# Performance work log

Measured on AMD Instinct MI355X. Metric: run time of the kernel, lower is better.

The kernel has to match this reference:

```python
import jax, jax.numpy as jnp
import numpy as np

POOL = 7        # output pooled size
SAMP = 2 * POOL # crop_and_resize sampling resolution (14)


def _bilinear_crop(feat, ys, xs):
    """feat [H,W,C]; ys,xs [N,S] sample coords in feature-map pixels -> [N,S,S,C]."""
    H, W, _ = feat.shape
    ys = jnp.clip(ys, 0.0, H - 1.0)
    xs = jnp.clip(xs, 0.0, W - 1.0)
    y0f = jnp.floor(ys); x0f = jnp.floor(xs)
    y0 = y0f.astype(jnp.int32); x0 = x0f.astype(jnp.int32)
    y1 = jnp.clip(y0 + 1, 0, H - 1); x1 = jnp.clip(x0 + 1, 0, W - 1)
    wy = (ys - y0f)[:, :, None, None]   # [N,S,1,1]
    wx = (xs - x0f)[:, None, :, None]   # [N,1,S,1]
    g = lambda yi, xi: feat[yi[:, :, None], xi[:, None, :]]  # [N,S,S,C]
    out = g(y0, x0) * (1 - wy) * (1 - wx)
    out = out + g(y0, x1) * (1 - wy) * wx
    out = out + g(y1, x0) * wy * (1 - wx)
    out = out + g(y1, x1) * wy * wx
    return out


def setup_inputs() -> dict:
    key = jax.random.key(0)
    k1, k2, k3, k4, k5 = jax.random.split(key, 5)
    Hf, Wf, C = 37, 50, 512
    N = 1000
    H_img, W_img = 600.0, 800.0
    inputs = jax.random.normal(k1, (1, Hf, Wf, C), dtype=jnp.float32)
    # random valid boxes (x1,y1,x2,y2) in image coords
    cx = jax.random.uniform(k2, (N,)) * W_img
    cy = jax.random.uniform(k3, (N,)) * H_img
    bw = jax.random.uniform(k4, (N,)) * 300.0 + 16.0
    bh = jax.random.uniform(k5, (N,)) * 300.0 + 16.0
    x1 = jnp.clip(cx - bw / 2, 0.0, W_img - 1.0)
    y1 = jnp.clip(cy - bh / 2, 0.0, H_img - 1.0)
    x2 = jnp.clip(cx + bw / 2, 0.0, W_img - 1.0)
    y2 = jnp.clip(cy + bh / 2, 0.0, H_img - 1.0)
    rois = jnp.stack([x1, y1, x2, y2], axis=1).astype(jnp.float32)
    im_size = jnp.array([600, 800], dtype=jnp.int32)  # (h, w)
    return {"inputs": inputs, "rois": rois, "im_size": im_size}


def reference(inputs, rois, im_size):
    feat = inputs[0]                       # [Hf, Wf, C]
    Hf, Wf, C = feat.shape
    h = im_size[0].astype(jnp.float32)
    w = im_size[1].astype(jnp.float32)
    # normalize boxes to [0,1] (y1, x1, y2, x2), as in roi_pool_tf
    ny1 = rois[:, 1] / h; nx1 = rois[:, 0] / w
    ny2 = rois[:, 3] / h; nx2 = rois[:, 2] / w
    # crop_and_resize sample grid (TF convention: endpoints at box corners)
    t = jnp.linspace(0.0, 1.0, SAMP, dtype=jnp.float32)          # [S]
    ys = (ny1[:, None] + (ny2 - ny1)[:, None] * t[None, :]) * (Hf - 1)  # [N,S]
    xs = (nx1[:, None] + (nx2 - nx1)[:, None] * t[None, :]) * (Wf - 1)  # [N,S]
    crops = _bilinear_crop(feat, ys, xs)   # [N,14,14,C]
    N = crops.shape[0]
    pooled = crops.reshape(N, POOL, 2, POOL, 2, C).max(axis=(2, 4))  # [N,7,7,C]
    return pooled
```

## Files before the change

kernel.cpp:

```cpp
#include <hip/hip_runtime.h>
#include <math.h>

#define HF 37
#define WF 50
#define CC 512
#define POOLD 7
#define SAMPD 14

typedef float nfloat4 __attribute__((ext_vector_type(4)));

__device__ __forceinline__ float4 lerp4(float4 a, float4 b, float t) {
    float4 r;
    r.x = a.x + t * (b.x - a.x);
    r.y = a.y + t * (b.y - a.y);
    r.z = a.z + t * (b.z - a.z);
    r.w = a.w + t * (b.w - a.w);
    return r;
}

__device__ __forceinline__ float4 max4(float4 a, float4 b) {
    float4 r;
    r.x = fmaxf(a.x, b.x);
    r.y = fmaxf(a.y, b.y);
    r.z = fmaxf(a.z, b.z);
    r.w = fmaxf(a.w, b.w);
    return r;
}

__device__ __forceinline__ void store_nt4(float* p, float4 v) {
    nfloat4 nv;
    nv.x = v.x; nv.y = v.y; nv.z = v.z; nv.w = v.w;
    __builtin_nontemporal_store(nv, (nfloat4*)p);
}

template <int RC>
__device__ __forceinline__ void loadcol(const float* __restrict__ pbase, int col,
                                        int ro0, int ro1, int ro2, int ro3,
                                        float wya, float wyb,
                                        float4& va, float4& vb) {
    const float* p = pbase + (size_t)col * CC;
    if (RC == 0) {
        float4 rA = *(const float4*)(p + ro0);
        float4 rB = *(const float4*)(p + ro1);
        va = lerp4(rA, rB, wya);
        vb = lerp4(rA, rB, wyb);
    } else if (RC == 1) {
        float4 rA = *(const float4*)(p + ro0);
        float4 rB = *(const float4*)(p + ro1);
        float4 rC = *(const float4*)(p + ro3);
        va = lerp4(rA, rB, wya);
        vb = lerp4(rB, rC, wyb);
    } else {
        float4 r0 = *(const float4*)(p + ro0);
        float4 r1 = *(const float4*)(p + ro1);
        float4 r2 = *(const float4*)(p + ro2);
        float4 r3 = *(const float4*)(p + ro3);
        va = lerp4(r0, r1, wya);
        vb = lerp4(r2, r3, wyb);
    }
}

template <int RC>
__device__ __forceinline__ void run_row(const float* __restrict__ pbase,
                                        float* __restrict__ obase,
                                        float nx1, float nx2,
                                        int ro0, int ro1, int ro2, int ro3,
                                        float wya, float wyb) {
    const float inv = 1.0f / (float)(SAMPD - 1);

    int pcol = -1000, ccol = -1000;
    float4 vap, vbp, vac, vbc;
    float4 m0 = make_float4(-INFINITY, -INFINITY, -INFINITY, -INFINITY);

    #pragma unroll 1
    for (int sx = 0; sx < SAMPD; ++sx) {
        float tx = (float)sx * inv;
        float xs = (nx1 + (nx2 - nx1) * tx) * (float)(WF - 1);
        xs = fminf(fmaxf(xs, 0.0f), (float)(WF - 1));
        float x0f = floorf(xs);
        float wx = xs - x0f;
        int c0 = __builtin_amdgcn_readfirstlane((int)x0f);
        int c1 = min(c0 + 1, WF - 1);

        if (c0 == ccol) {
            pcol = ccol; vap = vac; vbp = vbc;
            loadcol<RC>(pbase, c1, ro0, ro1, ro2, ro3, wya, wyb, vac, vbc);
            ccol = c1;
        } else if (c0 != pcol) {
            loadcol<RC>(pbase, c0, ro0, ro1, ro2, ro3, wya, wyb, vap, vbp);
            pcol = c0;
            loadcol<RC>(pbase, c1, ro0, ro1, ro2, ro3, wya, wyb, vac, vbc);
            ccol = c1;
        }

        float4 sa = lerp4(vap, vac, wx);
        float4 sb = lerp4(vbp, vbc, wx);
        float4 mm = max4(sa, sb);
        m0 = max4(m0, mm);

        if (sx & 1) {
            store_nt4(obase + (size_t)(sx >> 1) * CC, m0);
            m0 = make_float4(-INFINITY, -INFINITY, -INFINITY, -INFINITY);
        }
    }
}

__global__ __launch_bounds__(128, 4) void roipool_kernel(
    const float* __restrict__ feat,
    const float* __restrict__ rois,
    const int*   __restrict__ im_size,
    float*       __restrict__ out,
    int N)
{
    int bid = blockIdx.x;
    int n   = bid / POOLD;
    int py  = bid - n * POOLD;
    if (n >= N) return;

    float h = (float)im_size[0];
    float w = (float)im_size[1];
    float bx1 = rois[4 * n + 0];
    float by1 = rois[4 * n + 1];
    float bx2 = rois[4 * n + 2];
    float by2 = rois[4 * n + 3];
    float ny1 = by1 / h, nx1 = bx1 / w;
    float ny2 = by2 / h, nx2 = bx2 / w;

    const float inv = 1.0f / (float)(SAMPD - 1);

    float tya = (float)(2 * py) * inv;
    float tyb = (float)(2 * py + 1) * inv;
    float ysa = (ny1 + (ny2 - ny1) * tya) * (float)(HF - 1);
    float ysb = (ny1 + (ny2 - ny1) * tyb) * (float)(HF - 1);
    ysa = fminf(fmaxf(ysa, 0.0f), (float)(HF - 1));
    ysb = fminf(fmaxf(ysb, 0.0f), (float)(HF - 1));
    float y0fa = floorf(ysa);
    float y0fb = floorf(ysb);
    float wya = ysa - y0fa;
    float wyb = ysb - y0fb;
    int iya = __builtin_amdgcn_readfirstlane((int)y0fa);
    int iyb = __builtin_amdgcn_readfirstlane((int)y0fb);
    int iya1 = min(iya + 1, HF - 1);
    int iyb1 = min(iyb + 1, HF - 1);
    int ro0 = iya  * (WF * CC);
    int ro1 = iya1 * (WF * CC);
    int ro2 = iyb  * (WF * CC);
    int ro3 = iyb1 * (WF * CC);

    const float* pbase = feat + (size_t)threadIdx.x * 4;
    float* obase = out + ((size_t)(n * POOLD + py) * POOLD) * CC + (size_t)threadIdx.x * 4;

    if (ro2 == ro0) {
        run_row<0>(pbase, obase, nx1, nx2, ro0, ro1, ro2, ro3, wya, wyb);
    } else if (ro2 == ro1) {
        run_row<1>(pbase, obase, nx1, nx2, ro0, ro1, ro2, ro3, wya, wyb);
    } else {
        run_row<2>(pbase, obase, nx1, nx2, ro0, ro1, ro2, ro3, wya, wyb);
    }
}

extern "C" void kernel_launch(void* const* d_in, const int* in_sizes, int n_in,
                              void* d_out, int out_size, void* d_ws, size_t ws_size,
                              hipStream_t stream) {
    const float* feat    = (const float*)d_in[0];
    const float* rois    = (const float*)d_in[1];
    const int*   im_size = (const int*)d_in[2];
    float* out = (float*)d_out;

    int N = in_sizes[1] / 4;
    int nblocks = N * POOLD;
    roipool_kernel<<<nblocks, 128, 0, stream>>>(feat, rois, im_size, out, N);
}
```

Before: 124.0 us.

## Software-pipeline column loads and stage pooled outputs in LDS before storing

Restructures the per-row loop to walk feature columns from first to last, with double-buffered raw loads so the next column's global reads are issued before the current column is interpolated. Pooled results go to shared memory first and are written out with non-temporal stores at the end. The box is now read as one float4. The aim is to hide global load latency behind the lerp/max work. The cost is more registers and LDS traffic, and it may also load columns that no sample uses.

```diff
diff --git a/kernel.cpp b/kernel.cpp
--- a/kernel.cpp
+++ b/kernel.cpp
@@ -33,74 +33,102 @@
     __builtin_nontemporal_store(nv, (nfloat4*)p);
 }
 
+struct Raw { float4 a, b, c, d; };
+
 template <int RC>
-__device__ __forceinline__ void loadcol(const float* __restrict__ pbase, int col,
-                                        int ro0, int ro1, int ro2, int ro3,
-                                        float wya, float wyb,
-                                        float4& va, float4& vb) {
+__device__ __forceinline__ Raw loadraw(const float* __restrict__ pbase, int col,
+                                       int ro0, int ro1, int ro2, int ro3) {
     const float* p = pbase + (size_t)col * CC;
-    if (RC == 0) {
-        float4 rA = *(const float4*)(p + ro0);
-        float4 rB = *(const float4*)(p + ro1);
-        va = lerp4(rA, rB, wya);
-        vb = lerp4(rA, rB, wyb);
-    } else if (RC == 1) {
-        float4 rA = *(const float4*)(p + ro0);
-        float4 rB = *(const float4*)(p + ro1);
-        float4 rC = *(const float4*)(p + ro3);
-        va = lerp4(rA, rB, wya);
-        vb = lerp4(rB, rC, wyb);
-    } else {
-        float4 r0 = *(const float4*)(p + ro0);
-        float4 r1 = *(const float4*)(p + ro1);
-        float4 r2 = *(const float4*)(p + ro2);
-        float4 r3 = *(const float4*)(p + ro3);
-        va = lerp4(r0, r1, wya);
-        vb = lerp4(r2, r3, wyb);
-    }
+    Raw r;
+    r.a = *(const float4*)(p + ro0);
+    r.b = *(const float4*)(p + ro1);
+    if (RC == 1) { r.c = *(const float4*)(p + ro3); }
+    if (RC == 2) { r.c = *(const float4*)(p + ro2); r.d = *(const float4*)(p + ro3); }
+    return r;
+}
+
+template <int RC>
+__device__ __forceinline__ void vlerp(const Raw& r, float wya, float wyb,
+                                      float4& va, float4& vb) {
+    if (RC == 0)      { va = lerp4(r.a, r.b, wya); vb = lerp4(r.a, r.b, wyb); }
+    else if (RC == 1) { va = lerp4(r.a, r.b, wya); vb = lerp4(r.b, r.c, wyb); }
+    else              { va = lerp4(r.a, r.b, wya); vb = lerp4(r.c, r.d, wyb); }
 }
 
 template <int RC>
 __device__ __forceinline__ void run_row(const float* __restrict__ pbase,
-                                        float* __restrict__ obase,
-                                        float nx1, float nx2,
+                                        float4* __restrict__ lbase,
+                                        float nx1, float dx,
                                         int ro0, int ro1, int ro2, int ro3,
-                                        float wya, float wyb) {
-    const float inv = 1.0f / (float)(SAMPD - 1);
-
-    int pcol = -1000, ccol = -1000;
-    float4 vap, vbp, vac, vbc;
+                                        float wya, float wyb)
+{
+    const float inv    = 1.0f / (float)(SAMPD - 1);
+    const float wscale = (float)(WF - 1);
+
+    auto samp = [&](int sx, int& pc, float& w) {
+        float tx = (float)sx * inv;
+        float xs = fmaf(dx, tx, nx1) * wscale;
+        xs = fminf(fmaxf(xs, 0.0f), wscale);
+        float x0f = floorf(xs);
+        int ci = (int)x0f;
+        float wx = xs - x0f;
+        if (ci >= WF - 1) { pc = WF - 1; w = 1.0f; }
+        else              { pc = ci + 1; w = wx; }
+        pc = __builtin_amdgcn_readfirstlane(pc);
+    };
+
+    int pc0, pcl; float w0, wl;
+    samp(0, pc0, w0);
+    samp(SAMPD - 1, pcl, wl);
+    int cfirst = pc0 - 1;
+    int clast  = pcl;
+
+    Raw r0 = loadraw<RC>(pbase, cfirst, ro0, ro1, ro2, ro3);
+    Raw rA = loadraw<RC>(pbase, cfirst + 1, ro0, ro1, ro2, ro3);
+    Raw rB;
+    float4 vaP, vbP;
+    vlerp<RC>(r0, wya, wyb, vaP, vbP);
+
     float4 m0 = make_float4(-INFINITY, -INFINITY, -INFINITY, -INFINITY);
-
-    #pragma unroll 1
-    for (int sx = 0; sx < SAMPD; ++sx) {
-        float tx = (float)sx * inv;
-        float xs = (nx1 + (nx2 - nx1) * tx) * (float)(WF - 1);
-        xs = fminf(fmaxf(xs, 0.0f), (float)(WF - 1));
-        float x0f = floorf(xs);
-        float wx = xs - x0f;
-        int c0 = __builtin_amdgcn_readfirstlane((int)x0f);
-        int c1 = min(c0 + 1, WF - 1);
-
-        if (c0 == ccol) {
-            pcol = ccol; vap = vac; vbp = vbc;
-            loadcol<RC>(pbase, c1, ro0, ro1, ro2, ro3, wya, wyb, vac, vbc);
-            ccol = c1;
-        } else if (c0 != pcol) {
-            loadcol<RC>(pbase, c0, ro0, ro1, ro2, ro3, wya, wyb, vap, vbp);
-            pcol = c0;
-            loadcol<RC>(pbase, c1, ro0, ro1, ro2, ro3, wya, wyb, vac, vbc);
-            ccol = c1;
+    int sx = 0;
+    int c  = cfirst + 1;
+
+    auto consume = [&](float4 vaC, float4 vbC) {
+        for (;;) {
+            if (sx >= SAMPD) break;
+            int pc; float w;
+            samp(sx, pc, w);
+            if (pc > c) break;
+            float4 sa = lerp4(vaP, vaC, w);
+            float4 sb = lerp4(vbP, vbC, w);
+            m0 = max4(m0, max4(sa, sb));
+            if (sx & 1) {
+                lbase[(sx >> 1) * 128] = m0;
+                m0 = make_float4(-INFINITY, -INFINITY, -INFINITY, -INFINITY);
+            }
+            ++sx;
         }
-
-        float4 sa = lerp4(vap, vac, wx);
-        float4 sb = lerp4(vbp, vbc, wx);
-        float4 mm = max4(sa, sb);
-        m0 = max4(m0, mm);
-
-        if (sx & 1) {
-            store_nt4(obase + (size_t)(sx >> 1) * CC, m0);
-            m0 = make_float4(-INFINITY, -INFINITY, -INFINITY, -INFINITY);
+        vaP = vaC; vbP = vbC;
+    };
+
+    for (;;) {
+        {
+            int cn = min(c + 1, clast);
+            rB = loadraw<RC>(pbase, cn, ro0, ro1, ro2, ro3);
+            float4 vaC, vbC;
+            vlerp<RC>(rA, wya, wyb, vaC, vbC);
+            consume(vaC, vbC);
+            if (c == clast) return;
+            ++c;
+        }
+        {
+            int cn = min(c + 1, clast);
+            rA = loadraw<RC>(pbase, cn, ro0, ro1, ro2, ro3);
+            float4 vaC, vbC;
+            vlerp<RC>(rB, wya, wyb, vaC, vbC);
+            consume(vaC, vbC);
+            if (c == clast) return;
+            ++c;
         }
     }
 }
@@ -112,6 +140,8 @@
     float*       __restrict__ out,
     int N)
 {
+    __shared__ float4 lds_out[POOLD * 128];
+
     int bid = blockIdx.x;
     int n   = bid / POOLD;
     int py  = bid - n * POOLD;
@@ -119,12 +149,10 @@
 
     float h = (float)im_size[0];
     float w = (float)im_size[1];
-    float bx1 = rois[4 * n + 0];
-    float by1 = rois[4 * n + 1];
-    float bx2 = rois[4 * n + 2];
-    float by2 = rois[4 * n + 3];
-    float ny1 = by1 / h, nx1 = bx1 / w;
-    float ny2 = by2 / h, nx2 = bx2 / w;
+    float4 box = *(const float4*)(rois + 4 * n);
+    float ny1 = box.y / h, nx1 = box.x / w;
+    float ny2 = box.w / h, nx2 = box.z / w;
+    float dx = nx2 - nx1;
 
     const float inv = 1.0f / (float)(SAMPD - 1);
 
@@ -148,14 +176,21 @@
     int ro3 = iyb1 * (WF * CC);
 
     const float* pbase = feat + (size_t)threadIdx.x * 4;
+    float4* lbase = lds_out + threadIdx.x;
     float* obase = out + ((size_t)(n * POOLD + py) * POOLD) * CC + (size_t)threadIdx.x * 4;
 
     if (ro2 == ro0) {
-        run_row<0>(pbase, obase, nx1, nx2, ro0, ro1, ro2, ro3, wya, wyb);
+        run_row<0>(pbase, lbase, nx1, dx, ro0, ro1, ro2, ro3, wya, wyb);
     } else if (ro2 == ro1) {
-        run_row<1>(pbase, obase, nx1, nx2, ro0, ro1, ro2, ro3, wya, wyb);
+        run_row<1>(pbase, lbase, nx1, dx, ro0, ro1, ro2, ro3, wya, wyb);
     } else {
-        run_row<2>(pbase, obase, nx1, nx2, ro0, ro1, ro2, ro3, wya, wyb);
+        run_row<2>(pbase, lbase, nx1, dx, ro0, ro1, ro2, ro3, wya, wyb);
+    }
+
+    #pragma unroll
+    for (int p = 0; p < POOLD; ++p) {
+        float4 v = lbase[p * 128];
+        store_nt4(obase + (size_t)p * CC, v);
     }
 }
 
```

New measurement: 126.9 us. +2.3%, slower.

## Split channels into four slices per block with 64-thread float2 blocks

Applied to the files above, without the earlier changes.

Each (roi, pooled-row) block is now split into four blocks that each cover a 128-channel slice. Blocks shrink to one 64-thread wavefront using float2 loads and stores instead of float4, and the grid grows fourfold. The aim is more independent waves in flight to hide gather latency. In exchange, the per-block setup (roi load, y-coordinate math, x-column search) is repeated four times and each memory access is narrower.

```diff
diff --git a/kernel.cpp b/kernel.cpp
--- a/kernel.cpp
+++ b/kernel.cpp
@@ -7,56 +7,46 @@
 #define POOLD 7
 #define SAMPD 14
 
-typedef float nfloat4 __attribute__((ext_vector_type(4)));
+#define NSL 4
+#define SLICE (CC / NSL)
 
-__device__ __forceinline__ float4 lerp4(float4 a, float4 b, float t) {
-    float4 r;
-    r.x = a.x + t * (b.x - a.x);
-    r.y = a.y + t * (b.y - a.y);
-    r.z = a.z + t * (b.z - a.z);
-    r.w = a.w + t * (b.w - a.w);
-    return r;
+typedef float nfloat2 __attribute__((ext_vector_type(2)));
+
+__device__ __forceinline__ float2 lerp2(float2 a, float2 b, float t) {
+    float2 r; r.x = a.x + t * (b.x - a.x); r.y = a.y + t * (b.y - a.y); return r;
 }
-
-__device__ __forceinline__ float4 max4(float4 a, float4 b) {
-    float4 r;
-    r.x = fmaxf(a.x, b.x);
-    r.y = fmaxf(a.y, b.y);
-    r.z = fmaxf(a.z, b.z);
-    r.w = fmaxf(a.w, b.w);
-    return r;
+__device__ __forceinline__ float2 max2(float2 a, float2 b) {
+    float2 r; r.x = fmaxf(a.x, b.x); r.y = fmaxf(a.y, b.y); return r;
 }
-
-__device__ __forceinline__ void store_nt4(float* p, float4 v) {
-    nfloat4 nv;
-    nv.x = v.x; nv.y = v.y; nv.z = v.z; nv.w = v.w;
-    __builtin_nontemporal_store(nv, (nfloat4*)p);
+__device__ __forceinline__ void store_nt2(float* p, float2 v) {
+    nfloat2 nv; nv.x = v.x; nv.y = v.y;
+    __builtin_nontemporal_store(nv, (nfloat2*)p);
 }
 
 template <int RC>
 __device__ __forceinline__ void loadcol(const float* __restrict__ pbase, int col,
                                         int ro0, int ro1, int ro2, int ro3,
                                         float wya, float wyb,
-                                        float4& va, float4& vb) {
+                                        float2& va, float2& vb) {
     const float* p = pbase + (size_t)col * CC;
     if (RC == 0) {
-        float4 rA = *(const float4*)(p + ro0);
-        float4 rB = *(const float4*)(p + ro1);
-        va = lerp4(rA, rB, wya);
-        vb = lerp4(rA, rB, wyb);
+        float2 rA = *(const float2*)(p + ro0);
+        float2 rB = *(const float2*)(p + ro1);
+        va = lerp2(rA, rB, wya);
+        vb = lerp2(rA, rB, wyb);
     } else if (RC == 1) {
-        float4 rA = *(const float4*)(p + ro0);
-        float4 rB = *(const float4*)(p + ro1);
-        float4 rC = *(const float4*)(p + ro3);
-        va = lerp4(rA, rB, wya);
-        vb = lerp4(rB, rC, wyb);
+        float2 rA = *(const float2*)(p + ro0);
+        float2 rB = *(const float2*)(p + ro1);
+        float2 rC = *(const float2*)(p + ro3);
+        va = lerp2(rA, rB, wya);
+        vb = lerp2(rB, rC, wyb);
     } else {
-        float4 r0 = *(const float4*)(p + ro0);
-        float4 r1 = *(const float4*)(p + ro1);
-        float4 r2 = *(const float4*)(p + ro2);
-        float4 r3 = *(const float4*)(p + ro3);
-        va = lerp4(r0, r1, wya);
-        vb = lerp4(r2, r3, wyb);
+        float2 r0 = *(const float2*)(p + ro0);
+        float2 r1 = *(const float2*)(p + ro1);
+        float2 r2 = *(const float2*)(p + ro2);
+        float2 r3 = *(const float2*)(p + ro3);
+        va = lerp2(r0, r1, wya);
+        vb = lerp2(r2, r3, wyb);
     }
 }
 
@@ -69,8 +59,8 @@
     const float inv = 1.0f / (float)(SAMPD - 1);
 
     int pcol = -1000, ccol = -1000;
-    float4 vap, vbp, vac, vbc;
-    float4 m0 = make_float4(-INFINITY, -INFINITY, -INFINITY, -INFINITY);
+    float2 vap, vbp, vac, vbc;
+    float2 m0 = make_float2(-INFINITY, -INFINITY);
 
     #pragma unroll 1
     for (int sx = 0; sx < SAMPD; ++sx) {
@@ -93,19 +83,19 @@
             ccol = c1;
         }
 
-        float4 sa = lerp4(vap, vac, wx);
-        float4 sb = lerp4(vbp, vbc, wx);
-        float4 mm = max4(sa, sb);
-        m0 = max4(m0, mm);
+        float2 sa = lerp2(vap, vac, wx);
+        float2 sb = lerp2(vbp, vbc, wx);
+        float2 mm = max2(sa, sb);
+        m0 = max2(m0, mm);
 
         if (sx & 1) {
-            store_nt4(obase + (size_t)(sx >> 1) * CC, m0);
-            m0 = make_float4(-INFINITY, -INFINITY, -INFINITY, -INFINITY);
+            store_nt2(obase + (size_t)(sx >> 1) * CC, m0);
+            m0 = make_float2(-INFINITY, -INFINITY);
         }
     }
 }
 
-__global__ __launch_bounds__(128, 4) void roipool_kernel(
+__global__ __launch_bounds__(64, 8) void roipool_kernel(
     const float* __restrict__ feat,
     const float* __restrict__ rois,
     const int*   __restrict__ im_size,
@@ -113,18 +103,17 @@
     int N)
 {
     int bid = blockIdx.x;
-    int n   = bid / POOLD;
-    int py  = bid - n * POOLD;
+    int cs  = bid & (NSL - 1);
+    int rp  = bid >> 2;
+    int n   = rp / POOLD;
+    int py  = rp - n * POOLD;
     if (n >= N) return;
 
     float h = (float)im_size[0];
     float w = (float)im_size[1];
-    float bx1 = rois[4 * n + 0];
-    float by1 = rois[4 * n + 1];
-    float bx2 = rois[4 * n + 2];
-    float by2 = rois[4 * n + 3];
-    float ny1 = by1 / h, nx1 = bx1 / w;
-    float ny2 = by2 / h, nx2 = bx2 / w;
+    float4 box = *(const float4*)(rois + 4 * n);
+    float ny1 = box.y / h, nx1 = box.x / w;
+    float ny2 = box.w / h, nx2 = box.z / w;
 
     const float inv = 1.0f / (float)(SAMPD - 1);
 
@@ -147,8 +136,9 @@
     int ro2 = iyb  * (WF * CC);
     int ro3 = iyb1 * (WF * CC);
 
-    const float* pbase = feat + (size_t)threadIdx.x * 4;
-    float* obase = out + ((size_t)(n * POOLD + py) * POOLD) * CC + (size_t)threadIdx.x * 4;
+    const int choff = cs * SLICE + (int)threadIdx.x * 2;
+    const float* pbase = feat + choff;
+    float* obase = out + ((size_t)(n * POOLD + py) * POOLD) * CC + choff;
 
     if (ro2 == ro0) {
         run_row<0>(pbase, obase, nx1, nx2, ro0, ro1, ro2, ro3, wya, wyb);
@@ -168,6 +158,6 @@
     float* out = (float*)d_out;
 
     int N = in_sizes[1] / 4;
-    int nblocks = N * POOLD;
-    roipool_kernel<<<nblocks, 128, 0, stream>>>(feat, rois, im_size, out, N);
+    int nblocks = N * POOLD * NSL;
+    roipool_kernel<<<nblocks, 64, 0, stream>>>(feat, rois, im_size, out, N);
 }
```

Measured after the change: 130.7 us. +5.4%, slower.

## Convert feature map to fp16 in workspace and gather half-precision values

Applied to the files above, without the earlier changes.

Adds a pre-pass kernel that converts the fp32 feature map into an fp16 copy in the workspace. The main kernel then gathers fp16 values, 8 channels per thread with 64 threads per block, which halves the bytes read per bilinear sample. The fp32 kernel is kept as a fallback when the workspace is too small. This adds an extra launch and a full pass over the feature map, and it lowers the precision of the inputs, which could break the accuracy tolerance.

```diff
diff --git a/kernel.cpp b/kernel.cpp
--- a/kernel.cpp
+++ b/kernel.cpp
@@ -7,70 +7,89 @@
 #define POOLD 7
 #define SAMPD 14
 
-typedef float nfloat4 __attribute__((ext_vector_type(4)));
-
-__device__ __forceinline__ float4 lerp4(float4 a, float4 b, float t) {
-    float4 r;
-    r.x = a.x + t * (b.x - a.x);
-    r.y = a.y + t * (b.y - a.y);
-    r.z = a.z + t * (b.z - a.z);
-    r.w = a.w + t * (b.w - a.w);
-    return r;
-}
-
-__device__ __forceinline__ float4 max4(float4 a, float4 b) {
-    float4 r;
-    r.x = fmaxf(a.x, b.x);
-    r.y = fmaxf(a.y, b.y);
-    r.z = fmaxf(a.z, b.z);
-    r.w = fmaxf(a.w, b.w);
-    return r;
-}
-
-__device__ __forceinline__ void store_nt4(float* p, float4 v) {
-    nfloat4 nv;
-    nv.x = v.x; nv.y = v.y; nv.z = v.z; nv.w = v.w;
-    __builtin_nontemporal_store(nv, (nfloat4*)p);
+typedef float  nfloat4 __attribute__((ext_vector_type(4)));
+typedef _Float16 half8 __attribute__((ext_vector_type(8)));
+
+struct f8 { float v[8]; };
+
+__device__ __forceinline__ f8 cvt8(half8 h) {
+    f8 r;
+    #pragma unroll
+    for (int k = 0; k < 8; ++k) r.v[k] = (float)h[k];
+    return r;
+}
+__device__ __forceinline__ f8 lerp8(const f8& a, const f8& b, float t) {
+    f8 r;
+    #pragma unroll
+    for (int k = 0; k < 8; ++k) r.v[k] = a.v[k] + t * (b.v[k] - a.v[k]);
+    return r;
+}
+__device__ __forceinline__ f8 max8(const f8& a, const f8& b) {
+    f8 r;
+    #pragma unroll
+    for (int k = 0; k < 8; ++k) r.v[k] = fmaxf(a.v[k], b.v[k]);
+    return r;
+}
+__device__ __forceinline__ void store_nt8(float* p, const f8& m) {
+    nfloat4 a, b;
+    a.x = m.v[0]; a.y = m.v[1]; a.z = m.v[2]; a.w = m.v[3];
+    b.x = m.v[4]; b.y = m.v[5]; b.z = m.v[6]; b.w = m.v[7];
+    __builtin_nontemporal_store(a, (nfloat4*)p);
+    __builtin_nontemporal_store(b, (nfloat4*)(p + 4));
+}
+
+__global__ __launch_bounds__(256) void cvt_kernel(const float* __restrict__ in,
+                                                  _Float16* __restrict__ out,
+                                                  int total8) {
+    int i = blockIdx.x * blockDim.x + threadIdx.x;
+    if (i >= total8) return;
+    const float4* p = (const float4*)(in + (size_t)i * 8);
+    float4 a = p[0], b = p[1];
+    half8 h;
+    h[0] = (_Float16)a.x; h[1] = (_Float16)a.y; h[2] = (_Float16)a.z; h[3] = (_Float16)a.w;
+    h[4] = (_Float16)b.x; h[5] = (_Float16)b.y; h[6] = (_Float16)b.z; h[7] = (_Float16)b.w;
+    *(half8*)(out + (size_t)i * 8) = h;
 }
 
 template <int RC>
-__device__ __forceinline__ void loadcol(const float* __restrict__ pbase, int col,
-                                        int ro0, int ro1, int ro2, int ro3,
-                                        float wya, float wyb,
-                                        float4& va, float4& vb) {
-    const float* p = pbase + (size_t)col * CC;
+__device__ __forceinline__ void loadcol_h(const _Float16* __restrict__ pbase, int col,
+                                          int ro0, int ro1, int ro2, int ro3,
+                                          float wya, float wyb, f8& va, f8& vb) {
+    const _Float16* p = pbase + (size_t)col * CC;
     if (RC == 0) {
-        float4 rA = *(const float4*)(p + ro0);
-        float4 rB = *(const float4*)(p + ro1);
-        va = lerp4(rA, rB, wya);
-        vb = lerp4(rA, rB, wyb);
+        f8 rA = cvt8(*(const half8*)(p + ro0));
+        f8 rB = cvt8(*(const half8*)(p + ro1));
+        va = lerp8(rA, rB, wya);
+        vb = lerp8(rA, rB, wyb);
     } else if (RC == 1) {
-        float4 rA = *(const float4*)(p + ro0);
-        float4 rB = *(const float4*)(p + ro1);
-        float4 rC = *(const float4*)(p + ro3);
-        va = lerp4(rA, rB, wya);
-        vb = lerp4(rB, rC, wyb);
+        f8 rA = cvt8(*(const half8*)(p + ro0));
+        f8 rB = cvt8(*(const half8*)(p + ro1));
+        f8 rC = cvt8(*(const half8*)(p + ro3));
+        va = lerp8(rA, rB, wya);
+        vb = lerp8(rB, rC, wyb);
     } else {
-        float4 r0 = *(const float4*)(p + ro0);
-        float4 r1 = *(const float4*)(p + ro1);
-        float4 r2 = *(const float4*)(p + ro2);
-        float4 r3 = *(const float4*)(p + ro3);
-        va = lerp4(r0, r1, wya);
-        vb = lerp4(r2, r3, wyb);
+        f8 r0 = cvt8(*(const half8*)(p + ro0));
+        f8 r1 = cvt8(*(const half8*)(p + ro1));
+        f8 r2 = cvt8(*(const half8*)(p + ro2));
+        f8 r3 = cvt8(*(const half8*)(p + ro3));
+        va = lerp8(r0, r1, wya);
+        vb = lerp8(r2, r3, wyb);
     }
 }
 
 template <int RC>
-__device__ __forceinline__ void run_row(const float* __restrict__ pbase,
-                                        float* __restrict__ obase,
-                                        float nx1, float nx2,
-                                        int ro0, int ro1, int ro2, int ro3,
-                                        float wya, float wyb) {
+__device__ __forceinline__ void run_row_h(const _Float16* __restrict__ pbase,
+                                          float* __restrict__ obase,
+                                          float nx1, float nx2,
+                                          int ro0, int ro1, int ro2, int ro3,
+                                          float wya, float wyb) {
     const float inv = 1.0f / (float)(SAMPD - 1);
 
     int pcol = -1000, ccol = -1000;
-    float4 vap, vbp, vac, vbc;
-    float4 m0 = make_float4(-INFINITY, -INFINITY, -INFINITY, -INFINITY);
+    f8 vap, vbp, vac, vbc;
+    f8 m0;
+    #pragma unroll
+    for (int k = 0; k < 8; ++k) m0.v[k] = -INFINITY;
 
     #pragma unroll 1
     for (int sx = 0; sx < SAMPD; ++sx) {
@@ -84,29 +103,29 @@
 
         if (c0 == ccol) {
             pcol = ccol; vap = vac; vbp = vbc;
-            loadcol<RC>(pbase, c1, ro0, ro1, ro2, ro3, wya, wyb, vac, vbc);
+            loadcol_h<RC>(pbase, c1, ro0, ro1, ro2, ro3, wya, wyb, vac, vbc);
             ccol = c1;
         } else if (c0 != pcol) {
-            loadcol<RC>(pbase, c0, ro0, ro1, ro2, ro3, wya, wyb, vap, vbp);
+            loadcol_h<RC>(pbase, c0, ro0, ro1, ro2, ro3, wya, wyb, vap, vbp);
             pcol = c0;
-            loadcol<RC>(pbase, c1, ro0, ro1, ro2, ro3, wya, wyb, vac, vbc);
+            loadcol_h<RC>(pbase, c1, ro0, ro1, ro2, ro3, wya, wyb, vac, vbc);
             ccol = c1;
         }
 
-        float4 sa = lerp4(vap, vac, wx);
-        float4 sb = lerp4(vbp, vbc, wx);
-        float4 mm = max4(sa, sb);
-        m0 = max4(m0, mm);
+        f8 sa = lerp8(vap, vac, wx);
+        f8 sb = lerp8(vbp, vbc, wx);
+        m0 = max8(m0, max8(sa, sb));
 
         if (sx & 1) {
-            store_nt4(obase + (size_t)(sx >> 1) * CC, m0);
-            m0 = make_float4(-INFINITY, -INFINITY, -INFINITY, -INFINITY);
+            store_nt8(obase + (size_t)(sx >> 1) * CC, m0);
+            #pragma unroll
+            for (int k = 0; k < 8; ++k) m0.v[k] = -INFINITY;
         }
     }
 }
 
-__global__ __launch_bounds__(128, 4) void roipool_kernel(
-    const float* __restrict__ feat,
+__global__ __launch_bounds__(64, 8) void roipool_h_kernel(
+    const _Float16* __restrict__ hfeat,
     const float* __restrict__ rois,
     const int*   __restrict__ im_size,
     float*       __restrict__ out,
@@ -119,12 +138,9 @@
 
     float h = (float)im_size[0];
     float w = (float)im_size[1];
-    float bx1 = rois[4 * n + 0];
-    float by1 = rois[4 * n + 1];
-    float bx2 = rois[4 * n + 2];
-    float by2 = rois[4 * n + 3];
-    float ny1 = by1 / h, nx1 = bx1 / w;
-    float ny2 = by2 / h, nx2 = bx2 / w;
+    float4 box = *(const float4*)(rois + 4 * n);
+    float ny1 = box.y / h, nx1 = box.x / w;
+    float ny2 = box.w / h, nx2 = box.z / w;
 
     const float inv = 1.0f / (float)(SAMPD - 1);
 
@@ -147,16 +163,136 @@
     int ro2 = iyb  * (WF * CC);
     int ro3 = iyb1 * (WF * CC);
 
+    const _Float16* pbase = hfeat + (size_t)threadIdx.x * 8;
+    float* obase = out + ((size_t)(n * POOLD + py) * POOLD) * CC + (size_t)threadIdx.x * 8;
+
+    if (ro2 == ro0) {
+        run_row_h<0>(pbase, obase, nx1, nx2, ro0, ro1, ro2, ro3, wya, wyb);
+    } else if (ro2 == ro1) {
+        run_row_h<1>(pbase, obase, nx1, nx2, ro0, ro1, ro2, ro3, wya, wyb);
+    } else {
+        run_row_h<2>(pbase, obase, nx1, nx2, ro0, ro1, ro2, ro3, wya, wyb);
+    }
+}
+
+__device__ __forceinline__ float4 lerp4(float4 a, float4 b, float t) {
+    float4 r;
+    r.x = a.x + t * (b.x - a.x);
+    r.y = a.y + t * (b.y - a.y);
+    r.z = a.z + t * (b.z - a.z);
+    r.w = a.w + t * (b.w - a.w);
+    return r;
+}
+__device__ __forceinline__ float4 max4(float4 a, float4 b) {
+    float4 r;
+    r.x = fmaxf(a.x, b.x); r.y = fmaxf(a.y, b.y);
+    r.z = fmaxf(a.z, b.z); r.w = fmaxf(a.w, b.w);
+    return r;
+}
+__device__ __forceinline__ void store_nt4(float* p, float4 v) {
+    nfloat4 nv; nv.x = v.x; nv.y = v.y; nv.z = v.z; nv.w = v.w;
+    __builtin_nontemporal_store(nv, (nfloat4*)p);
+}
+
+template <int RC>
+__device__ __forceinline__ void loadcol_f(const float* __restrict__ pbase, int col,
+                                          int ro0, int ro1, int ro2, int ro3,
+                                          float wya, float wyb, float4& va, float4& vb) {
+    const float* p = pbase + (size_t)col * CC;
+    if (RC == 0) {
+        float4 rA = *(const float4*)(p + ro0);
+        float4 rB = *(const float4*)(p + ro1);
+        va = lerp4(rA, rB, wya); vb = lerp4(rA, rB, wyb);
+    } else if (RC == 1) {
+        float4 rA = *(const float4*)(p + ro0);
+        float4 rB = *(const float4*)(p + ro1);
+        float4 rC = *(const float4*)(p + ro3);
+        va = lerp4(rA, rB, wya); vb = lerp4(rB, rC, wyb);
+    } else {
+        float4 r0 = *(const float4*)(p + ro0);
+        float4 r1 = *(const float4*)(p + ro1);
+        float4 r2 = *(const float4*)(p + ro2);
+        float4 r3 = *(const float4*)(p + ro3);
+        va = lerp4(r0, r1, wya); vb = lerp4(r2, r3, wyb);
+    }
+}
+
+template <int RC>
+__device__ __forceinline__ void run_row_f(const float* __restrict__ pbase,
+                                          float* __restrict__ obase,
+                                          float nx1, float nx2,
+                                          int ro0, int ro1, int ro2, int ro3,
+                                          float wya, float wyb) {
+    const float inv = 1.0f / (float)(SAMPD - 1);
+    int pcol = -1000, ccol = -1000;
+    float4 vap, vbp, vac, vbc;
+    float4 m0 = make_float4(-INFINITY, -INFINITY, -INFINITY, -INFINITY);
+    #pragma unroll 1
+    for (int sx = 0; sx < SAMPD; ++sx) {
+        float tx = (float)sx * inv;
+        float xs = (nx1 + (nx2 - nx1) * tx) * (float)(WF - 1);
+        xs = fminf(fmaxf(xs, 0.0f), (float)(WF - 1));
+        float x0f = floorf(xs);
+        float wx = xs - x0f;
+        int c0 = __builtin_amdgcn_readfirstlane((int)x0f);
+        int c1 = min(c0 + 1, WF - 1);
+        if (c0 == ccol) {
+            pcol = ccol; vap = vac; vbp = vbc;
+            loadcol_f<RC>(pbase, c1, ro0, ro1, ro2, ro3, wya, wyb, vac, vbc);
+            ccol = c1;
+        } else if (c0 != pcol) {
+            loadcol_f<RC>(pbase, c0, ro0, ro1, ro2, ro3, wya, wyb, vap, vbp);
+            pcol = c0;
+            loadcol_f<RC>(pbase, c1, ro0, ro1, ro2, ro3, wya, wyb, vac, vbc);
+            ccol = c1;
+        }
+        float4 sa = lerp4(vap, vac, wx);
+        float4 sb = lerp4(vbp, vbc, wx);
+        m0 = max4(m0, max4(sa, sb));
+        if (sx & 1) {
+            store_nt4(obase + (size_t)(sx >> 1) * CC, m0);
+            m0 = make_float4(-INFINITY, -INFINITY, -INFINITY, -INFINITY);
+        }
+    }
+}
+
+__global__ __launch_bounds__(128, 4) void roipool_f_kernel(
+    const float* __restrict__ feat, const float* __restrict__ rois,
+    const int* __restrict__ im_size, float* __restrict__ out, int N)
+{
+    int bid = blockIdx.x;
+    int n   = bid / POOLD;
+    int py  = bid - n * POOLD;
+    if (n >= N) return;
+
+    float h = (float)im_size[0];
+    float w = (float)im_size[1];
+    float4 box = *(const float4*)(rois + 4 * n);
+    float ny1 = box.y / h, nx1 = box.x / w;
+    float ny2 = box.w / h, nx2 = box.z / w;
+    const float inv = 1.0f / (float)(SAMPD - 1);
+
+    float tya = (float)(2 * py) * inv;
+    float tyb = (float)(2 * py + 1) * inv;
+    float ysa = (ny1 + (ny2 - ny1) * tya) * (float)(HF - 1);
+    float ysb = (ny1 + (ny2 - ny1) * tyb) * (float)(HF - 1);
+    ysa = fminf(fmaxf(ysa, 0.0f), (float)(HF - 1));
+    ysb = fminf(fmaxf(ysb, 0.0f), (float)(HF - 1));
+    float y0fa = floorf(ysa), y0fb = floorf(ysb);
+    float wya = ysa - y0fa, wyb = ysb - y0fb;
+    int iya = __builtin_amdgcn_readfirstlane((int)y0fa);
+    int iyb = __builtin_amdgcn_readfirstlane((int)y0fb);
+    int iya1 = min(iya + 1, HF - 1);
+    int iyb1 = min(iyb + 1, HF - 1);
+    int ro0 = iya * (WF * CC), ro1 = iya1 * (WF * CC);
+    int ro2 = iyb * (WF * CC), ro3 = iyb1 * (WF * CC);
+
     const float* pbase = feat + (size_t)threadIdx.x * 4;
     float* obase = out + ((size_t)(n * POOLD + py) * POOLD) * CC + (size_t)threadIdx.x * 4;
 
-    if (ro2 == ro0) {
-        run_row<0>(pbase, obase, nx1, nx2, ro0, ro1, ro2, ro3, wya, wyb);
-    } else if (ro2 == ro1) {
-        run_row<1>(pbase, obase, nx1, nx2, ro0, ro1, ro2, ro3, wya, wyb);
-    } else {
-        run_row<2>(pbase, obase, nx1, nx2, ro0, ro1, ro2, ro3, wya, wyb);
-    }
+    if (ro2 == ro0)      run_row_f<0>(pbase, obase, nx1, nx2, ro0, ro1, ro2, ro3, wya, wyb);
+    else if (ro2 == ro1) run_row_f<1>(pbase, obase, nx1, nx2, ro0, ro1, ro2, ro3, wya, wyb);
+    else                 run_row_f<2>(pbase, obase, nx1, nx2, ro0, ro1, ro2, ro3, wya, wyb);
 }
 
 extern "C" void kernel_launch(void* const* d_in, const int* in_sizes, int n_in,
@@ -169,5 +305,14 @@
 
     int N = in_sizes[1] / 4;
     int nblocks = N * POOLD;
-    roipool_kernel<<<nblocks, 128, 0, stream>>>(feat, rois, im_size, out, N);
-}
+
+    const size_t need = (size_t)HF * WF * CC * sizeof(_Float16);
+    if (d_ws != nullptr && ws_size >= need) {
+        _Float16* hbuf = (_Float16*)d_ws;
+        int total8 = (HF * WF * CC) / 8;
+        cvt_kernel<<<(total8 + 255) / 256, 256, 0, stream>>>(feat, hbuf, total8);
+        roipool_h_kernel<<<nblocks, 64, 0, stream>>>(hbuf, rois, im_size, out, N);
+    } else {
+        roipool_f_kernel<<<nblocks, 128, 0, stream>>>(feat, rois, im_size, out, N);
+    }
+}
```

After: 139.8 us. 12.7% more time.
